# Optimization experiments

Measured on AMD Instinct MI355X. Metric: run time of the kernel, lower is better.

## Reference

```python
import jax, jax.numpy as jnp
import numpy as np

N_CLASS, N_SUPPORT, N_QUERY = 64, 5, 64
D_IN, C, WIN = 1024, 128, 5
D = C * WIN * WIN  # 3200, fine-encoder output dim


def setup_inputs() -> dict:
    key = jax.random.key(0)
    ks = jax.random.split(key, 6)
    s = 0.02  # weight init scale
    return {
        "xs": jax.random.normal(ks[0], (N_CLASS, N_SUPPORT, D_IN), jnp.float32),
        "xq": jax.random.normal(ks[1], (N_CLASS, N_QUERY, D_IN), jnp.float32),
        "W_share": jax.random.normal(ks[2], (D_IN, D), jnp.float32) * s,
        "b_share": jnp.zeros((D,), jnp.float32),
        "W_att": jax.random.normal(ks[3], (C, C), jnp.float32) * s,
        "b_att": jnp.zeros((C,), jnp.float32),
        "W_fine": jax.random.normal(ks[4], (D, D), jnp.float32) * s,
        "b_fine": jnp.zeros((D,), jnp.float32),
    }


def reference(xs, xq, W_share, b_share, W_att, b_att, W_fine, b_fine):
    n_class, n_support = xs.shape[0], xs.shape[1]
    n_query = xq.shape[1]
    ns = n_class * n_support

    # concat support + query, run shared encoder
    x = jnp.concatenate([xs.reshape(ns, -1), xq.reshape(n_class * n_query, -1)], axis=0)
    z_share = jax.nn.relu(x @ W_share + b_share)            # [N, D]
    z4 = z_share.reshape(-1, C, WIN, WIN)

    # attention head: spatial mean -> linear -> per-channel logits
    z_att = z4.mean(axis=(2, 3)) @ W_att + b_att            # [N, C]

    diag_c = jax.nn.softmax(z_att[:ns].mean(axis=0)) * C    # [C]
    w = jnp.repeat(diag_c, WIN * WIN)                       # [D] diagonal of learned metric

    # fine encoder (flatten + linear)
    z = z_share @ W_fine + b_fine                           # [N, D]
    z_proto = z[:ns].reshape(n_class, n_support, -1).mean(axis=1)  # [n_class, D]
    zq = z[ns:]                                             # [n, D]

    # attentionMetric with diagonal metric == weighted squared distance:
    # dists[i,j] = sum_d w_d (zq_i - proto_j)^2, expanded to avoid the n*m*d diff tensor
    q2 = (zq * zq) @ w                                      # [n]
    p2 = (z_proto * z_proto) @ w                            # [m]
    cross = (zq * w) @ z_proto.T                            # [n, m]
    dists = q2[:, None] + p2[None, :] - 2.0 * cross         # [n, m]

    log_p_y = jax.nn.log_softmax(-dists, axis=1).reshape(n_class, n_query, n_class)
    target = jnp.arange(n_class)
    tgt = jnp.broadcast_to(target[:, None, None], (n_class, n_query, 1))
    loss_val = -jnp.take_along_axis(log_p_y, tgt, axis=2).mean()
    y_hat = jnp.argmax(log_p_y, axis=2)
    acc_val = (y_hat == target[:, None]).astype(jnp.float32).mean()
    return loss_val, acc_val
```

## Files before the change

### kernel.cpp

```cpp
#include <hip/hip_runtime.h>
#include <math.h>

#define N_CLASS 64
#define N_SUPPORT 5
#define N_QUERY 64
#define D_IN 1024
#define C_CH 128
#define WIN 5
#define D_FEAT 3200
#define NS 320
#define NQ 4096
#define M_ROWS 4416
#define M_PAD 4480

#define ZP_SLICE  (N_CLASS * D_FEAT)
#define GT_SLICE  (128 * D_FEAT)
#define CR_SLICE  (NQ * 128)
#define NKS       10
#define LOSS_BLKS (NQ / 4)

#define PREP_X   4480
#define PREP_WS  3200
#define CONV_WF  10000

#define WS_SCALE    64.0f
#define WS_INVSCALE 0.015625f

typedef __bf16 bf16x8 __attribute__((ext_vector_type(8)));
typedef __bf16 bf16x4 __attribute__((ext_vector_type(4)));
typedef float floatx4 __attribute__((ext_vector_type(4)));
typedef __attribute__((address_space(1))) const void* gptr_t;
typedef __attribute__((address_space(3))) void* lptr_t;

__device__ __forceinline__ float waveReduceSum(float v) {
    for (int off = 32; off > 0; off >>= 1) v += __shfl_xor(v, off, 64);
    return v;
}

__global__ __launch_bounds__(256) void prep_kernel(const float* __restrict__ xs,
                                                   const float* __restrict__ xq,
                                                   const float* __restrict__ W_share,
                                                   unsigned char* __restrict__ Xf8,
                                                   unsigned char* __restrict__ Wsf8)
{
    __shared__ float tile[32][33];
    const int b = blockIdx.x;
    const int t = threadIdx.x;

    if (b < PREP_X) {
        const int e = (b * 256 + t) * 4;
        const int row = e >> 10;
        const int col = e & 1023;
        float4 v = make_float4(0.f, 0.f, 0.f, 0.f);
        if (row < NS)          v = *(const float4*)(xs + (size_t)row * D_IN + col);
        else if (row < M_ROWS) v = *(const float4*)(xq + (size_t)(row - NS) * D_IN + col);
        int p = __builtin_amdgcn_cvt_pk_fp8_f32(v.x, v.y, 0, false);
        p     = __builtin_amdgcn_cvt_pk_fp8_f32(v.z, v.w, p, true);
        const int ocol = col ^ (((row >> 3) & 1) << 3);
        *(int*)(Xf8 + (size_t)row * D_IN + ocol) = p;
        return;
    }
    const int tx = t & 31;
    const int ty = t >> 5;
    const int tb = b - PREP_X;
    const int n0 = (tb % 100) * 32;
    const int k0 = (tb / 100) * 32;
#pragma unroll
    for (int i = ty; i < 32; i += 8)
        tile[i][tx] = W_share[(size_t)(k0 + i) * D_FEAT + n0 + tx];
    __syncthreads();
#pragma unroll
    for (int i = ty; i < 32; i += 8) {
        const int p = __builtin_amdgcn_cvt_pk_fp8_f32(tile[tx][i] * WS_SCALE, 0.f,
                                                      0, false);
        const int n = n0 + i;
        const int k = (k0 + tx) ^ (((n >> 3) & 1) << 3);
        Wsf8[(size_t)n * D_IN + k] = (unsigned char)(p & 0xff);
    }
}

__global__ __launch_bounds__(256) void gemm_fp8(const unsigned char* __restrict__ A,
                                                const unsigned char* __restrict__ Bt,
                                                const float* __restrict__ bias,
                                                __bf16* __restrict__ out_bf,
                                                int N, int strideK, int kIters,
                                                int Mout, int nbx, int nby)
{
    __shared__ __align__(16) char smem[32768];

    int bx, by;
    {
        const int b  = blockIdx.x;
        const int fg = nbx >> 3;
        const int full = fg * 8 * nby;
        if (b < full) {
            const int g = b / (8 * nby);
            const int r = b - g * 8 * nby;
            bx = g * 8 + (r & 7);
            by = r >> 3;
        } else {
            const int rem = nbx - fg * 8;
            const int r = b - full;
            bx = fg * 8 + r % rem;
            by = r / rem;
        }
    }

    const int t    = threadIdx.x;
    const int lane = t & 63;
    const int w    = t >> 6;
    const int wm   = w >> 1;
    const int wn   = w & 1;
    const int bm   = by * 128;
    const int bn   = bx * 128;

    const int q    = lane >> 4;
    const int r16  = lane & 15;
    const int b7   = r16 & 7;
    const int hs   = (r16 >> 3) & 1;

    const int smRow  = t >> 3;
    const int sgk16  = ((t & 7) ^ ((t >> 3) & 7)) * 16;

    floatx4 acc[4][4] = {};

    for (int ki = 0; ki < kIters; ++ki) {
        const int k0 = ki * 128;
        __syncthreads();
#pragma unroll
        for (int i = 0; i < 4; ++i) {
            const unsigned char* ga = A  + (size_t)(bm + i * 32 + smRow) * strideK
                                         + k0 + sgk16;
            const unsigned char* gb = Bt + (size_t)(bn + i * 32 + smRow) * strideK
                                         + k0 + sgk16;
            char* la = smem +         i * 4096 + t * 16;
            char* lb = smem + 16384 + i * 4096 + t * 16;
            __builtin_amdgcn_global_load_lds((gptr_t)ga, (lptr_t)la, 16, 0, 0);
            __builtin_amdgcn_global_load_lds((gptr_t)gb, (lptr_t)lb, 16, 0, 0);
        }
        __syncthreads();

#pragma unroll
        for (int s32 = 0; s32 < 4; ++s32) {
            const int qq = s32 * 4 + q;
            const int colOff = (((qq >> 1) ^ b7) * 16) + (((qq & 1) ^ hs) * 8);
            long av[4], bv[4];
#pragma unroll
            for (int mi = 0; mi < 4; ++mi)
                av[mi] = *(const long*)(smem
                            + (wm * 64 + mi * 16 + r16) * 128 + colOff);
#pragma unroll
            for (int ni = 0; ni < 4; ++ni)
                bv[ni] = *(const long*)(smem + 16384
                            + (wn * 64 + ni * 16 + r16) * 128 + colOff);
#pragma unroll
            for (int mi = 0; mi < 4; ++mi)
#pragma unroll
                for (int ni = 0; ni < 4; ++ni)
                    acc[mi][ni] = __builtin_amdgcn_mfma_f32_16x16x32_fp8_fp8(
                        av[mi], bv[ni], acc[mi][ni], 0, 0, 0);
        }
    }

#pragma unroll
    for (int ni = 0; ni < 4; ++ni) {
        const int col = bn + wn * 64 + ni * 16 + r16;
        const float bcol = bias[col];
#pragma unroll
        for (int mi = 0; mi < 4; ++mi) {
#pragma unroll
            for (int reg = 0; reg < 4; ++reg) {
                const int row = bm + wm * 64 + mi * 16 + q * 4 + reg;
                if (row < Mout) {
                    float v = acc[mi][ni][reg] * WS_INVSCALE + bcol;
                    v = fmaxf(v, 0.f);
                    out_bf[(size_t)row * N + col] = (__bf16)v;
                }
            }
        }
    }
}

__global__ __launch_bounds__(256) void gemm_bf16(const __bf16* __restrict__ A,
                                                 const __bf16* __restrict__ Bt,
                                                 const float* __restrict__ bias,
                                                 __bf16* __restrict__ out_bf,
                                                 float* __restrict__ out_f32,
                                                 int N, int strideK, int kIters,
                                                 int Mout, int relu, int sliceStride,
                                                 int nbx, int nby)
{
    __shared__ __align__(16) char smem[32768];

    int bx, by, ks;
    {
        const int nbxy = nbx * nby;
        ks = blockIdx.x / nbxy;
        const int b = blockIdx.x - ks * nbxy;
        const int fg = nbx >> 3;
        const int full = fg * 8 * nby;
        if (b < full) {
            const int g = b / (8 * nby);
            const int r = b - g * 8 * nby;
            bx = g * 8 + (r & 7);
            by = r >> 3;
        } else {
            const int rem = nbx - fg * 8;
            const int r = b - full;
            bx = fg * 8 + r % rem;
            by = r / rem;
        }
    }

    const int t    = threadIdx.x;
    const int lane = t & 63;
    const int w    = t >> 6;
    const int wm   = w >> 1;
    const int wn   = w & 1;
    const int bm   = by * 128;
    const int bn   = bx * 128;

    const int q    = lane >> 4;
    const int r16  = lane & 15;
    const int sw   = (r16 >> 1) & 3;
    const int cA   = (q ^ sw) * 8;

    const int srow   = w * 16 + (lane >> 2);
    const int sglob8 = (((lane & 3) ^ ((lane >> 3) & 3))) * 8;

    const int kBase = ks * kIters * 64;
    floatx4 acc[4][4] = {};

    for (int ki = 0; ki < kIters; ++ki) {
        const int k0 = kBase + ki * 64;
        __syncthreads();
#pragma unroll
        for (int s = 0; s < 2; ++s) {
#pragma unroll
            for (int j = 0; j < 2; ++j) {
                const __bf16* ga = A  + (size_t)(bm + j * 64 + srow) * strideK
                                      + k0 + s * 32 + sglob8;
                const __bf16* gb = Bt + (size_t)(bn + j * 64 + srow) * strideK
                                      + k0 + s * 32 + sglob8;
                char* la = smem +         s * 8192 + (j * 256 + w * 64) * 16;
                char* lb = smem + 16384 + s * 8192 + (j * 256 + w * 64) * 16;
                __builtin_amdgcn_global_load_lds((gptr_t)ga, (lptr_t)la, 16, 0, 0);
                __builtin_amdgcn_global_load_lds((gptr_t)gb, (lptr_t)lb, 16, 0, 0);
            }
        }
        __syncthreads();

#pragma unroll
        for (int s = 0; s < 2; ++s) {
            const __bf16* sAe = (const __bf16*)(smem +         s * 8192);
            const __bf16* sBe = (const __bf16*)(smem + 16384 + s * 8192);
            bf16x8 av[4], bv[4];
#pragma unroll
            for (int mi = 0; mi < 4; ++mi)
                av[mi] = *(const bf16x8*)(sAe + ((wm * 64 + mi * 16 + r16) * 32 + cA));
#pragma unroll
            for (int ni = 0; ni < 4; ++ni)
                bv[ni] = *(const bf16x8*)(sBe + ((wn * 64 + ni * 16 + r16) * 32 + cA));
#pragma unroll
            for (int mi = 0; mi < 4; ++mi)
#pragma unroll
                for (int ni = 0; ni < 4; ++ni)
                    acc[mi][ni] = __builtin_amdgcn_mfma_f32_16x16x32_bf16(
                        av[mi], bv[ni], acc[mi][ni], 0, 0, 0);
        }
    }

#pragma unroll
    for (int ni = 0; ni < 4; ++ni) {
        const int col = bn + wn * 64 + ni * 16 + r16;
        const float bcol = sliceStride ? 0.f : bias[col];
#pragma unroll
        for (int mi = 0; mi < 4; ++mi) {
#pragma unroll
            for (int reg = 0; reg < 4; ++reg) {
                const int row = bm + wm * 64 + mi * 16 + q * 4 + reg;
                if (row < Mout) {
                    if (sliceStride) {
                        out_f32[(size_t)ks * sliceStride + (size_t)row * N + col] =
                            acc[mi][ni][reg];
                    } else {
                        float v = acc[mi][ni][reg] + bcol;
                        if (relu) v = fmaxf(v, 0.f);
                        if (out_f32) out_f32[(size_t)row * N + col] = v;
                        else         out_bf [(size_t)row * N + col] = (__bf16)v;
                    }
                }
            }
        }
    }
}

__global__ __launch_bounds__(256) void ut_conv_kernel(const __bf16* __restrict__ z_share,
                                                      const float* __restrict__ W_fine,
                                                      __bf16* __restrict__ u,
                                                      float* __restrict__ upool,
                                                      __bf16* __restrict__ Wfb,
                                                      __bf16* __restrict__ WfTb)
{
    __shared__ __align__(16) char smem_u[D_FEAT * 4];
    const int b = blockIdx.x;
    const int t = threadIdx.x;

    if (b >= 128) {
        float (*tile)[33] = (float(*)[33])smem_u;
        const int tb = b - 128;
        const int tx = t & 31;
        const int ty = t >> 5;
        const int n0 = (tb % 100) * 32;
        const int k0 = (tb / 100) * 32;
#pragma unroll
        for (int i = ty; i < 32; i += 8) {
            const float v = W_fine[(size_t)(k0 + i) * D_FEAT + n0 + tx];
            Wfb[(size_t)(k0 + i) * D_FEAT + n0 + tx] = (__bf16)v;
            tile[i][tx] = v;
        }
        __syncthreads();
#pragma unroll
        for (int i = ty; i < 32; i += 8)
            WfTb[(size_t)(n0 + i) * D_FEAT + k0 + tx] = (__bf16)tile[tx][i];
        return;
    }

    float* srow_ = (float*)smem_u;
    const int p = b;
    if (p >= N_CLASS) {
        for (int k = t; k < D_FEAT; k += 256) u[(size_t)p * D_FEAT + k] = (__bf16)0.f;
        return;
    }
    const __bf16* base = z_share + (size_t)(p * N_SUPPORT) * D_FEAT;
    for (int k = t; k < D_FEAT; k += 256) {
        float s = 0.f;
#pragma unroll
        for (int ss = 0; ss < N_SUPPORT; ++ss) s += (float)base[(size_t)ss * D_FEAT + k];
        s *= (1.0f / N_SUPPORT);
        u[(size_t)p * D_FEAT + k] = (__bf16)s;
        srow_[k] = s;
    }
    __syncthreads();
    if (t < C_CH) {
        float pool = 0.f;
#pragma unroll
        for (int win = 0; win < 25; ++win) pool += srow_[t * 25 + win];
        upool[(size_t)p * C_CH + t] = pool;
    }
}

__global__ __launch_bounds__(128) void att2_kernel(const float* __restrict__ upool,
                                                   const float* __restrict__ W_att,
                                                   const float* __restrict__ b_att,
                                                   float* __restrict__ wvec)
{
    __shared__ float s_pm[C_CH];
    __shared__ float s_att[C_CH];
    __shared__ float s_diag[C_CH];
    const int c = threadIdx.x;
    float a = 0.f;
    for (int p = 0; p < N_CLASS; ++p) a += upool[(size_t)p * C_CH + c];
    s_pm[c] = a * (1.0f / (N_CLASS * 25));
    __syncthreads();
    float acc = b_att[c];
    for (int k = 0; k < C_CH; ++k) acc += s_pm[k] * W_att[k * C_CH + c];
    s_att[c] = acc;
    __syncthreads();
    float m = -INFINITY;
    for (int k = 0; k < C_CH; ++k) m = fmaxf(m, s_att[k]);
    float s = 0.f;
    for (int k = 0; k < C_CH; ++k) s += expf(s_att[k] - m);
    s_diag[c] = expf(acc - m) / s * (float)C_CH;
    __syncthreads();
    for (int j = c; j < D_FEAT; j += C_CH) wvec[j] = s_diag[j / 25];
}

__global__ __launch_bounds__(256) void y_kernel(const float* __restrict__ zp_part,
                                                const float* __restrict__ wv,
                                                const float* __restrict__ bf,
                                                __bf16* __restrict__ y,
                                                float* __restrict__ p2,
                                                float* __restrict__ cvec)
{
    __shared__ float s_red2[8];
    const int p = blockIdx.x;
    const int t = threadIdx.x;
    if (p >= N_CLASS) {
        for (int j = t; j < D_FEAT; j += 256) y[(size_t)p * D_FEAT + j] = (__bf16)0.f;
        return;
    }
    float s2 = 0.f, sc = 0.f;
    for (int j = t; j < D_FEAT; j += 256) {
        float zpf = bf[j];
#pragma unroll
        for (int ss = 0; ss < NKS; ++ss)
            zpf += zp_part[(size_t)ss * ZP_SLICE + (size_t)p * D_FEAT + j];
        const float wj = wv[j];
        y[(size_t)p * D_FEAT + j] = (__bf16)(wj * zpf);
        s2 += wj * zpf * zpf;
        sc += bf[j] * wj * zpf;
    }
    s2 = waveReduceSum(s2);
    sc = waveReduceSum(sc);
    const int lane = t & 63, wid = t >> 6;
    if (lane == 0) { s_red2[wid] = s2; s_red2[4 + wid] = sc; }
    __syncthreads();
    if (t == 0) {
        p2[p]   = s_red2[0] + s_red2[1] + s_red2[2] + s_red2[3];
        cvec[p] = s_red2[4] + s_red2[5] + s_red2[6] + s_red2[7];
    }
}

__global__ __launch_bounds__(256) void gtsum_kernel(const float* __restrict__ gp,
                                                    __bf16* __restrict__ Gt)
{
    const int i4 = blockIdx.x * 256 + threadIdx.x;
    if (i4 >= GT_SLICE / 4) return;
    float4 s = make_float4(0.f, 0.f, 0.f, 0.f);
#pragma unroll
    for (int ss = 0; ss < NKS; ++ss) {
        const float4 v = *(const float4*)(gp + (size_t)ss * GT_SLICE + i4 * 4);
        s.x += v.x; s.y += v.y; s.z += v.z; s.w += v.w;
    }
    bf16x4 o = { (__bf16)s.x, (__bf16)s.y, (__bf16)s.z, (__bf16)s.w };
    *(bf16x4*)(Gt + (size_t)i4 * 4) = o;
}

__global__ __launch_bounds__(256) void loss_kernel(const float* __restrict__ cross_part,
                                                   const float* __restrict__ p2,
                                                   const float* __restrict__ cvec,
                                                   float* __restrict__ lpart)
{
    __shared__ float s_l[4], s_a[4];
    const int t = threadIdx.x;
    const int lane = t & 63, wid = t >> 6;
    const int i = blockIdx.x * 4 + wid;
    float cr = 0.f;
#pragma unroll
    for (int ss = 0; ss < NKS; ++ss)
        cr += cross_part[(size_t)ss * CR_SLICE + (size_t)i * 128 + lane];
    const float neg = 2.0f * (cr + cvec[lane]) - p2[lane];
    float m = neg;
    for (int off = 32; off > 0; off >>= 1) m = fmaxf(m, __shfl_xor(m, off, 64));
    float e = expf(neg - m);
    float ssum = e;
    for (int off = 32; off > 0; off >>= 1) ssum += __shfl_xor(ssum, off, 64);
    const float lse = m + logf(ssum);
    const int tcls = i >> 6;
    const float negt = __shfl(neg, tcls, 64);
    float v = -neg; int bi = lane;
    for (int off = 32; off > 0; off >>= 1) {
        const float ov = __shfl_xor(v, off, 64);
        const int   oi = __shfl_xor(bi, off, 64);
        if (ov < v || (ov == v && oi < bi)) { v = ov; bi = oi; }
    }
    if (lane == 0) { s_l[wid] = lse - negt; s_a[wid] = (bi == tcls) ? 1.0f : 0.0f; }
    __syncthreads();
    if (t == 0) {
        lpart[blockIdx.x]             = s_l[0] + s_l[1] + s_l[2] + s_l[3];
        lpart[LOSS_BLKS + blockIdx.x] = s_a[0] + s_a[1] + s_a[2] + s_a[3];
    }
}

__global__ __launch_bounds__(256) void writeout_kernel(const float* __restrict__ lpart,
                                                       float* __restrict__ out)
{
    __shared__ float s_red2[8];
    const int t = threadIdx.x;
    float l = 0.f, a = 0.f;
    for (int k = t; k < LOSS_BLKS; k += 256) {
        l += lpart[k];
        a += lpart[LOSS_BLKS + k];
    }
    l = waveReduceSum(l);
    a = waveReduceSum(a);
    const int lane = t & 63, wid = t >> 6;
    if (lane == 0) { s_red2[wid] = l; s_red2[4 + wid] = a; }
    __syncthreads();
    if (t == 0) {
        out[0] = (s_red2[0] + s_red2[1] + s_red2[2] + s_red2[3]) * (1.0f / NQ);
        out[1] = (s_red2[4] + s_red2[5] + s_red2[6] + s_red2[7]) * (1.0f / NQ);
    }
}

extern "C" void kernel_launch(void* const* d_in, const int* in_sizes, int n_in,
                              void* d_out, int out_size, void* d_ws, size_t ws_size,
                              hipStream_t stream)
{
    const float* xs      = (const float*)d_in[0];
    const float* xq      = (const float*)d_in[1];
    const float* W_share = (const float*)d_in[2];
    const float* b_share = (const float*)d_in[3];
    const float* W_att   = (const float*)d_in[4];
    const float* b_att   = (const float*)d_in[5];
    const float* W_fine  = (const float*)d_in[6];
    const float* b_fine  = (const float*)d_in[7];
    float* out = (float*)d_out;

    char* ws = (char*)d_ws;
    unsigned char* Xf8  = (unsigned char*)(ws);
    unsigned char* Wsf8 = (unsigned char*)(ws + 4587520);
    __bf16* Zsb     = (__bf16*)(ws +   7864320);
    __bf16* Wfb     = (__bf16*)(ws +  36536320);
    __bf16* WfTb    = (__bf16*)(ws +  57016320);
    float*  arena   = (float*) (ws +  77496320);
    float*  upool   = arena;
    float*  zp_part = arena;
    float*  gt_part = arena;
    float*  cr_part = arena;
    __bf16* ub      = (__bf16*)(ws +  98467840);
    __bf16* yb      = (__bf16*)(ws +  99287040);
    __bf16* Gt      = (__bf16*)(ws + 100106240);
    float*  wv      = (float*) (ws + 100925440);
    float*  p2v     = (float*) (ws + 100938240);
    float*  cvec    = (float*) (ws + 100938752);
    float*  lpart   = (float*) (ws + 100939264);

    prep_kernel<<<PREP_X + PREP_WS, 256, 0, stream>>>(xs, xq, W_share, Xf8, Wsf8);

    gemm_fp8<<<(D_FEAT / 128) * (M_PAD / 128), 256, 0, stream>>>(
        Xf8, Wsf8, b_share, Zsb,
        D_FEAT, D_IN, D_IN / 128, M_ROWS, D_FEAT / 128, M_PAD / 128);

    ut_conv_kernel<<<128 + CONV_WF, 256, 0, stream>>>(Zsb, W_fine, ub, upool,
                                                      Wfb, WfTb);
    att2_kernel<<<1, C_CH, 0, stream>>>(upool, W_att, b_att, wv);

    gemm_bf16<<<25 * NKS, 256, 0, stream>>>(
        ub, WfTb, nullptr, nullptr, zp_part,
        D_FEAT, D_FEAT, 5, N_CLASS, 0, ZP_SLICE, 25, 1);

    y_kernel<<<128, 256, 0, stream>>>(zp_part, wv, b_fine, yb, p2v, cvec);

    gemm_bf16<<<25 * NKS, 256, 0, stream>>>(
        yb, Wfb, nullptr, nullptr, gt_part,
        D_FEAT, D_FEAT, 5, 128, 0, GT_SLICE, 25, 1);

    gtsum_kernel<<<(GT_SLICE / 4 + 255) / 256, 256, 0, stream>>>(gt_part, Gt);

    gemm_bf16<<<32 * NKS, 256, 0, stream>>>(
        Zsb + (size_t)NS * D_FEAT, Gt, nullptr, nullptr, cr_part,
        128, D_FEAT, 5, NQ, 0, CR_SLICE, 1, 32);

    loss_kernel<<<LOSS_BLKS, 256, 0, stream>>>(cr_part, p2v, cvec, lpart);

    writeout_kernel<<<1, 256, 0, stream>>>(lpart, out);
}
```

Before: 256.6 us.

## Rewrite FP8 shared-encoder GEMM as 256x256 tiles with 4-stage LDS pipeline

Replaces the 128x128 single-buffered FP8 GEMM with a 512-thread, 256x256-tile kernel that keeps four K-stages in 128KB of LDS. Global-to-LDS loads are prefetched three stages ahead and overlapped with MFMA work, using barriers, explicit waitcnts and raised wave priority around the MFMA bursts. To support this, M and N are padded to multiples of 256, the FP8 swizzle pattern changes, and the prep kernel zero-fills the extra weight rows. The aim is to raise data reuse and hide load latency in the largest GEMM. The cost is a large LDS footprint that limits occupancy, plus extra padded work.

```diff
diff --git a/kernel.cpp b/kernel.cpp
--- a/kernel.cpp
+++ b/kernel.cpp
@@ -11,7 +11,8 @@
 #define NS 320
 #define NQ 4096
 #define M_ROWS 4416
-#define M_PAD 4480
+#define M_PAD8 4608
+#define N_PAD8 3328
 
 #define ZP_SLICE  (N_CLASS * D_FEAT)
 #define GT_SLICE  (128 * D_FEAT)
@@ -19,12 +20,27 @@
 #define NKS       10
 #define LOSS_BLKS (NQ / 4)
 
-#define PREP_X   4480
+#define PREP_X   4608
 #define PREP_WS  3200
+#define PREP_WZ  128
 #define CONV_WF  10000
 
 #define WS_SCALE    64.0f
 #define WS_INVSCALE 0.015625f
+
+#define WS_XF8      0u
+#define WS_WSF8     4718592u
+#define WS_ZSB      8126464u
+#define WS_WFB      36388864u
+#define WS_WFTB     56868864u
+#define WS_ARENA    77348864u
+#define WS_UB       98320384u
+#define WS_YB       99139584u
+#define WS_GT       99958784u
+#define WS_WV       100777984u
+#define WS_P2       100790784u
+#define WS_CVEC     100791296u
+#define WS_LPART    100791808u
 
 typedef __bf16 bf16x8 __attribute__((ext_vector_type(8)));
 typedef __bf16 bf16x4 __attribute__((ext_vector_type(4)));
@@ -56,125 +72,140 @@
         else if (row < M_ROWS) v = *(const float4*)(xq + (size_t)(row - NS) * D_IN + col);
         int p = __builtin_amdgcn_cvt_pk_fp8_f32(v.x, v.y, 0, false);
         p     = __builtin_amdgcn_cvt_pk_fp8_f32(v.z, v.w, p, true);
-        const int ocol = col ^ (((row >> 3) & 1) << 3);
+        const int ocol = col ^ (((row >> 1) & 1) << 3);
         *(int*)(Xf8 + (size_t)row * D_IN + ocol) = p;
         return;
     }
-    const int tx = t & 31;
-    const int ty = t >> 5;
-    const int tb = b - PREP_X;
-    const int n0 = (tb % 100) * 32;
-    const int k0 = (tb / 100) * 32;
-#pragma unroll
-    for (int i = ty; i < 32; i += 8)
-        tile[i][tx] = W_share[(size_t)(k0 + i) * D_FEAT + n0 + tx];
-    __syncthreads();
-#pragma unroll
-    for (int i = ty; i < 32; i += 8) {
-        const int p = __builtin_amdgcn_cvt_pk_fp8_f32(tile[tx][i] * WS_SCALE, 0.f,
-                                                      0, false);
-        const int n = n0 + i;
-        const int k = (k0 + tx) ^ (((n >> 3) & 1) << 3);
-        Wsf8[(size_t)n * D_IN + k] = (unsigned char)(p & 0xff);
-    }
-}
-
-__global__ __launch_bounds__(256) void gemm_fp8(const unsigned char* __restrict__ A,
-                                                const unsigned char* __restrict__ Bt,
-                                                const float* __restrict__ bias,
-                                                __bf16* __restrict__ out_bf,
-                                                int N, int strideK, int kIters,
-                                                int Mout, int nbx, int nby)
-{
-    __shared__ __align__(16) char smem[32768];
-
-    int bx, by;
-    {
-        const int b  = blockIdx.x;
-        const int fg = nbx >> 3;
-        const int full = fg * 8 * nby;
-        if (b < full) {
-            const int g = b / (8 * nby);
-            const int r = b - g * 8 * nby;
-            bx = g * 8 + (r & 7);
-            by = r >> 3;
-        } else {
-            const int rem = nbx - fg * 8;
-            const int r = b - full;
-            bx = fg * 8 + r % rem;
-            by = r / rem;
-        }
-    }
+    if (b < PREP_X + PREP_WS) {
+        const int tx = t & 31;
+        const int ty = t >> 5;
+        const int tb = b - PREP_X;
+        const int n0 = (tb % 100) * 32;
+        const int k0 = (tb / 100) * 32;
+#pragma unroll
+        for (int i = ty; i < 32; i += 8)
+            tile[i][tx] = W_share[(size_t)(k0 + i) * D_FEAT + n0 + tx];
+        __syncthreads();
+#pragma unroll
+        for (int i = ty; i < 32; i += 8) {
+            const int p = __builtin_amdgcn_cvt_pk_fp8_f32(tile[tx][i] * WS_SCALE, 0.f,
+                                                          0, false);
+            const int n = n0 + i;
+            const int k = (k0 + tx) ^ (((n >> 1) & 1) << 3);
+            Wsf8[(size_t)n * D_IN + k] = (unsigned char)(p & 0xff);
+        }
+        return;
+    }
+    const int r = b - (PREP_X + PREP_WS);
+    ((int*)(Wsf8 + (size_t)(3200 + r) * D_IN))[t] = 0;
+}
+
+__global__ __launch_bounds__(512, 2) void gemm_fp8_8p(const unsigned char* __restrict__ A,
+                                                      const unsigned char* __restrict__ Bt,
+                                                      const float* __restrict__ bias,
+                                                      __bf16* __restrict__ out_bf)
+{
+    __shared__ __align__(16) unsigned char smem[131072];
 
     const int t    = threadIdx.x;
     const int lane = t & 63;
     const int w    = t >> 6;
-    const int wm   = w >> 1;
-    const int wn   = w & 1;
-    const int bm   = by * 128;
-    const int bn   = bx * 128;
+    const int wm   = w >> 2;
+    const int wn   = w & 3;
+
+    const int bx = blockIdx.x % 13;
+    const int by = blockIdx.x / 13;
+    const int bm = by * 256;
+    const int bn = bx * 256;
 
     const int q    = lane >> 4;
     const int r16  = lane & 15;
-    const int b7   = r16 & 7;
-    const int hs   = (r16 >> 3) & 1;
-
-    const int smRow  = t >> 3;
-    const int sgk16  = ((t & 7) ^ ((t >> 3) & 7)) * 16;
-
-    floatx4 acc[4][4] = {};
-
-    for (int ki = 0; ki < kIters; ++ki) {
-        const int k0 = ki * 128;
-        __syncthreads();
-#pragma unroll
-        for (int i = 0; i < 4; ++i) {
-            const unsigned char* ga = A  + (size_t)(bm + i * 32 + smRow) * strideK
-                                         + k0 + sgk16;
-            const unsigned char* gb = Bt + (size_t)(bn + i * 32 + smRow) * strideK
-                                         + k0 + sgk16;
-            char* la = smem +         i * 4096 + t * 16;
-            char* lb = smem + 16384 + i * 4096 + t * 16;
-            __builtin_amdgcn_global_load_lds((gptr_t)ga, (lptr_t)la, 16, 0, 0);
-            __builtin_amdgcn_global_load_lds((gptr_t)gb, (lptr_t)lb, 16, 0, 0);
-        }
-        __syncthreads();
-
-#pragma unroll
-        for (int s32 = 0; s32 < 4; ++s32) {
-            const int qq = s32 * 4 + q;
-            const int colOff = (((qq >> 1) ^ b7) * 16) + (((qq & 1) ^ hs) * 8);
-            long av[4], bv[4];
-#pragma unroll
-            for (int mi = 0; mi < 4; ++mi)
-                av[mi] = *(const long*)(smem
-                            + (wm * 64 + mi * 16 + r16) * 128 + colOff);
+    const int m3   = (r16 >> 1) & 7;
+    const int off0 = (q ^ m3) * 8;
+
+    const int rowA = (wm * 128 + r16) * 64;
+    const int rowB = (wn * 64 + r16) * 64;
+
+    const int srow  = t >> 2;
+    const int sunit = 16 * ((t & 3) ^ ((srow >> 2) & 3));
+
+    auto stage_a = [&](int uu) {
+        const unsigned char* g = A + (size_t)(bm + srow) * D_IN + uu * 64 + sunit;
+        unsigned char* l = smem + (uu & 3) * 32768 + t * 16;
+        __builtin_amdgcn_global_load_lds((gptr_t)g,            (lptr_t)l,          16, 0, 0);
+        __builtin_amdgcn_global_load_lds((gptr_t)(g + 131072), (lptr_t)(l + 8192), 16, 0, 0);
+    };
+    auto stage_b = [&](int uu) {
+        const unsigned char* g = Bt + (size_t)(bn + srow) * D_IN + uu * 64 + sunit;
+        unsigned char* l = smem + (uu & 3) * 32768 + 16384 + t * 16;
+        __builtin_amdgcn_global_load_lds((gptr_t)g,            (lptr_t)l,          16, 0, 0);
+        __builtin_amdgcn_global_load_lds((gptr_t)(g + 131072), (lptr_t)(l + 8192), 16, 0, 0);
+    };
+
+    floatx4 acc[8][4] = {};
+    long av[8], bv[4];
+
+    auto ld_frags = [&](const unsigned char* sa, int o) {
+        const unsigned char* sb = sa + 16384;
+#pragma unroll
+        for (int mi = 0; mi < 8; ++mi) av[mi] = *(const long*)(sa + rowA + mi * 1024 + o);
+#pragma unroll
+        for (int ni = 0; ni < 4; ++ni) bv[ni] = *(const long*)(sb + rowB + ni * 1024 + o);
+    };
+    auto do_mfma = [&]() {
+        __builtin_amdgcn_s_barrier();
+        asm volatile("s_waitcnt lgkmcnt(0)" ::: "memory");
+        __builtin_amdgcn_s_setprio(1);
+#pragma unroll
+        for (int mi = 0; mi < 8; ++mi)
 #pragma unroll
             for (int ni = 0; ni < 4; ++ni)
-                bv[ni] = *(const long*)(smem + 16384
-                            + (wn * 64 + ni * 16 + r16) * 128 + colOff);
-#pragma unroll
-            for (int mi = 0; mi < 4; ++mi)
-#pragma unroll
-                for (int ni = 0; ni < 4; ++ni)
-                    acc[mi][ni] = __builtin_amdgcn_mfma_f32_16x16x32_fp8_fp8(
-                        av[mi], bv[ni], acc[mi][ni], 0, 0, 0);
-        }
+                acc[mi][ni] = __builtin_amdgcn_mfma_f32_16x16x32_fp8_fp8(
+                    av[mi], bv[ni], acc[mi][ni], 0, 0, 0);
+        __builtin_amdgcn_s_setprio(0);
+        __builtin_amdgcn_s_barrier();
+    };
+
+    stage_a(0); stage_b(0);
+    stage_a(1); stage_b(1);
+    stage_a(2); stage_b(2);
+
+    for (int u = 0; u < 13; ++u) {
+        const unsigned char* sa = smem + (u & 3) * 32768;
+        asm volatile("s_waitcnt vmcnt(8)" ::: "memory");
+        __builtin_amdgcn_s_barrier();
+        ld_frags(sa, off0);
+        stage_a(u + 3);
+        do_mfma();
+        ld_frags(sa, off0 ^ 32);
+        stage_b(u + 3);
+        do_mfma();
+    }
+    asm volatile("s_waitcnt vmcnt(0)" ::: "memory");
+    __builtin_amdgcn_s_barrier();
+    for (int u = 13; u < 16; ++u) {
+        const unsigned char* sa = smem + (u & 3) * 32768;
+        ld_frags(sa, off0);
+        do_mfma();
+        ld_frags(sa, off0 ^ 32);
+        do_mfma();
     }
 
 #pragma unroll
     for (int ni = 0; ni < 4; ++ni) {
         const int col = bn + wn * 64 + ni * 16 + r16;
-        const float bcol = bias[col];
-#pragma unroll
-        for (int mi = 0; mi < 4; ++mi) {
-#pragma unroll
-            for (int reg = 0; reg < 4; ++reg) {
-                const int row = bm + wm * 64 + mi * 16 + q * 4 + reg;
-                if (row < Mout) {
-                    float v = acc[mi][ni][reg] * WS_INVSCALE + bcol;
-                    v = fmaxf(v, 0.f);
-                    out_bf[(size_t)row * N + col] = (__bf16)v;
+        if (col < D_FEAT) {
+            const float bcol = bias[col];
+#pragma unroll
+            for (int mi = 0; mi < 8; ++mi) {
+#pragma unroll
+                for (int reg = 0; reg < 4; ++reg) {
+                    const int row = bm + wm * 128 + mi * 16 + q * 4 + reg;
+                    if (row < M_ROWS) {
+                        float v = acc[mi][ni][reg] * WS_INVSCALE + bcol;
+                        v = fmaxf(v, 0.f);
+                        out_bf[(size_t)row * D_FEAT + col] = (__bf16)v;
+                    }
                 }
             }
         }
@@ -499,29 +530,28 @@
     float* out = (float*)d_out;
 
     char* ws = (char*)d_ws;
-    unsigned char* Xf8  = (unsigned char*)(ws);
-    unsigned char* Wsf8 = (unsigned char*)(ws + 4587520);
-    __bf16* Zsb     = (__bf16*)(ws +   7864320);
-    __bf16* Wfb     = (__bf16*)(ws +  36536320);
-    __bf16* WfTb    = (__bf16*)(ws +  57016320);
-    float*  arena   = (float*) (ws +  77496320);
+    unsigned char* Xf8  = (unsigned char*)(ws + WS_XF8);
+    unsigned char* Wsf8 = (unsigned char*)(ws + WS_WSF8);
+    __bf16* Zsb     = (__bf16*)(ws + WS_ZSB);
+    __bf16* Wfb     = (__bf16*)(ws + WS_WFB);
+    __bf16* WfTb    = (__bf16*)(ws + WS_WFTB);
+    float*  arena   = (float*) (ws + WS_ARENA);
     float*  upool   = arena;
     float*  zp_part = arena;
     float*  gt_part = arena;
     float*  cr_part = arena;
-    __bf16* ub      = (__bf16*)(ws +  98467840);
-    __bf16* yb      = (__bf16*)(ws +  99287040);
-    __bf16* Gt      = (__bf16*)(ws + 100106240);
-    float*  wv      = (float*) (ws + 100925440);
-    float*  p2v     = (float*) (ws + 100938240);
-    float*  cvec    = (float*) (ws + 100938752);
-    float*  lpart   = (float*) (ws + 100939264);
-
-    prep_kernel<<<PREP_X + PREP_WS, 256, 0, stream>>>(xs, xq, W_share, Xf8, Wsf8);
-
-    gemm_fp8<<<(D_FEAT / 128) * (M_PAD / 128), 256, 0, stream>>>(
-        Xf8, Wsf8, b_share, Zsb,
-        D_FEAT, D_IN, D_IN / 128, M_ROWS, D_FEAT / 128, M_PAD / 128);
+    __bf16* ub      = (__bf16*)(ws + WS_UB);
+    __bf16* yb      = (__bf16*)(ws + WS_YB);
+    __bf16* Gt      = (__bf16*)(ws + WS_GT);
+    float*  wv      = (float*) (ws + WS_WV);
+    float*  p2v     = (float*) (ws + WS_P2);
+    float*  cvec    = (float*) (ws + WS_CVEC);
+    float*  lpart   = (float*) (ws + WS_LPART);
+
+    prep_kernel<<<PREP_X + PREP_WS + PREP_WZ, 256, 0, stream>>>(xs, xq, W_share,
+                                                                Xf8, Wsf8);
+
+    gemm_fp8_8p<<<18 * 13, 512, 0, stream>>>(Xf8, Wsf8, b_share, Zsb);
 
     ut_conv_kernel<<<128 + CONV_WF, 256, 0, stream>>>(Zsb, W_fine, ub, upool,
                                                       Wfb, WfTb);
```

Result: no change. 253.7 us (-1.1%).
